# Optimization experiments

Measured on AMD Instinct MI355X. Metric: run time of the kernel, lower is better.

The kernel has to match this reference:

```python
import jax, jax.numpy as jnp
import numpy as np

# Config constants (mirror Qwen3_5TextConfig)
H = 1024        # hidden_size
I = 512         # moe_intermediate_size
IS = 2048       # shared_expert_intermediate_size
E = 16          # num_experts
TOP_K = 4       # num_experts_per_tok
NORM_TOPK = True
B, S = 1, 1024


def setup_inputs() -> dict:
    key = jax.random.key(0)
    ks = jax.random.split(key, 10)
    s = 0.02
    return {
        "hidden_states": jax.random.normal(ks[0], (B, S, H), jnp.float32),
        "w_router": (jax.random.normal(ks[1], (H, E), jnp.float32) * s),
        # stacked expert weights; Linear(H->I) stored as [E, H, I] for einsum
        "w_gate": (jax.random.normal(ks[2], (E, H, I), jnp.float32) * s),
        "w_up": (jax.random.normal(ks[3], (E, H, I), jnp.float32) * s),
        "w_down": (jax.random.normal(ks[4], (E, I, H), jnp.float32) * s),
        # shared expert (dense MLP)
        "ws_gate": (jax.random.normal(ks[5], (H, IS), jnp.float32) * s),
        "ws_up": (jax.random.normal(ks[6], (H, IS), jnp.float32) * s),
        "ws_down": (jax.random.normal(ks[7], (IS, H), jnp.float32) * s),
        "w_shared_gate": (jax.random.normal(ks[8], (H, 1), jnp.float32) * s),
    }


def reference(hidden_states, w_router, w_gate, w_up, w_down,
              ws_gate, ws_up, ws_down, w_shared_gate):
    b, sl, hd = hidden_states.shape
    x = hidden_states.reshape(-1, hd)              # [T, H]
    T = x.shape[0]

    # --- router: softmax in fp32, top-k, optional renormalization ---
    router_logits = x @ w_router                   # [T, E]
    probs = jax.nn.softmax(router_logits.astype(jnp.float32), axis=-1)
    top_w, top_i = jax.lax.top_k(probs, TOP_K)     # [T, K]
    if NORM_TOPK:
        top_w = top_w / top_w.sum(axis=-1, keepdims=True)
    # dense per-token expert weights (zeros off the top-k)
    dense_w = jnp.zeros((T, E), x.dtype).at[jnp.arange(T)[:, None], top_i].set(
        top_w.astype(x.dtype))                     # [T, E]

    # --- expert MLPs (SwiGLU), computed for all experts then masked-combined ---
    g = jnp.einsum('th,ehi->tei', x, w_gate)       # [T, E, I]
    u = jnp.einsum('th,ehi->tei', x, w_up)         # [T, E, I]
    expert_out = jnp.einsum('tei,eih->teh', jax.nn.silu(g) * u, w_down)  # [T, E, H]
    moe_out = jnp.einsum('te,teh->th', dense_w, expert_out)             # [T, H]

    # --- shared expert + sigmoid gate ---
    shared = (jax.nn.silu(x @ ws_gate) * (x @ ws_up)) @ ws_down          # [T, H]
    shared_gate = jax.nn.sigmoid(x @ w_shared_gate)                      # [T, 1]
    out = (moe_out + shared_gate * shared).reshape(b, sl, hd)
    return out, router_logits
```

## Files before the change

### kernel.cpp

```cpp
#include <hip/hip_runtime.h>
#include <hip/hip_bf16.h>

#define T_ 1024
#define H_ 1024
#define I_ 512
#define IS_ 2048
#define E_ 16

typedef __attribute__((ext_vector_type(8))) short short8;
typedef __attribute__((ext_vector_type(4))) float f32x4;

__device__ __forceinline__ unsigned short f2bf(float f) {
  unsigned u = __builtin_bit_cast(unsigned, f);
  unsigned r = (u + 0x7fffu + ((u >> 16) & 1u)) >> 16;
  return (unsigned short)r;
}

__device__ __forceinline__ void gload16(const void* g, void* l) {
  __builtin_amdgcn_global_load_lds(
      (const __attribute__((address_space(1))) unsigned int*)g,
      (__attribute__((address_space(3))) unsigned int*)l, 16, 0, 0);
}

__device__ __forceinline__ void transpose_cstrip(
    const float* __restrict__ src, unsigned short* __restrict__ dst,
    int C, int Rf, int r_start, int n0, int nch) {
  __shared__ unsigned short tile[2][64 * 66];
  int tid = threadIdx.x;
  int c = (tid & 15) << 2;
  int r0 = (tid >> 4) << 2;
  int orr = tid >> 2;
  int ks = (tid & 3) << 4;
  const float* sp0 = src + (long)(r_start + r0) * C + n0 + c;
  unsigned short* dbase = dst + (long)(n0 + orr) * Rf + r_start + ks;

  float4 va[4], vb[4];
#pragma unroll
  for (int r = 0; r < 4; r++) va[r] = *(const float4*)(sp0 + (long)r * C);

  for (int t = 0; t < nch; t += 2) {
    {
      const float* sp = sp0 + (long)(t + 1) * 64 * C;
#pragma unroll
      for (int r = 0; r < 4; r++) vb[r] = *(const float4*)(sp + (long)r * C);
    }
    {
      unsigned short* tb = &tile[0][0];
      ushort4 w;
      w = (ushort4){f2bf(va[0].x), f2bf(va[1].x), f2bf(va[2].x), f2bf(va[3].x)};
      *(ushort4*)&tb[(c + 0) * 66 + r0] = w;
      w = (ushort4){f2bf(va[0].y), f2bf(va[1].y), f2bf(va[2].y), f2bf(va[3].y)};
      *(ushort4*)&tb[(c + 1) * 66 + r0] = w;
      w = (ushort4){f2bf(va[0].z), f2bf(va[1].z), f2bf(va[2].z), f2bf(va[3].z)};
      *(ushort4*)&tb[(c + 2) * 66 + r0] = w;
      w = (ushort4){f2bf(va[0].w), f2bf(va[1].w), f2bf(va[2].w), f2bf(va[3].w)};
      *(ushort4*)&tb[(c + 3) * 66 + r0] = w;
      asm volatile("s_waitcnt lgkmcnt(0)" ::: "memory");
      __builtin_amdgcn_sched_barrier(0);
      __builtin_amdgcn_s_barrier();
      __builtin_amdgcn_sched_barrier(0);
      uint4 o0 = *(const uint4*)&tb[orr * 66 + ks];
      uint4 o1 = *(const uint4*)&tb[orr * 66 + ks + 8];
      unsigned short* d = dbase + (long)t * 64;
      *(uint4*)d = o0;
      *(uint4*)(d + 8) = o1;
    }
    if (t + 2 < nch) {
      const float* sp = sp0 + (long)(t + 2) * 64 * C;
#pragma unroll
      for (int r = 0; r < 4; r++) va[r] = *(const float4*)(sp + (long)r * C);
    }
    {
      unsigned short* tb = &tile[1][0];
      ushort4 w;
      w = (ushort4){f2bf(vb[0].x), f2bf(vb[1].x), f2bf(vb[2].x), f2bf(vb[3].x)};
      *(ushort4*)&tb[(c + 0) * 66 + r0] = w;
      w = (ushort4){f2bf(vb[0].y), f2bf(vb[1].y), f2bf(vb[2].y), f2bf(vb[3].y)};
      *(ushort4*)&tb[(c + 1) * 66 + r0] = w;
      w = (ushort4){f2bf(vb[0].z), f2bf(vb[1].z), f2bf(vb[2].z), f2bf(vb[3].z)};
      *(ushort4*)&tb[(c + 2) * 66 + r0] = w;
      w = (ushort4){f2bf(vb[0].w), f2bf(vb[1].w), f2bf(vb[2].w), f2bf(vb[3].w)};
      *(ushort4*)&tb[(c + 3) * 66 + r0] = w;
      asm volatile("s_waitcnt lgkmcnt(0)" ::: "memory");
      __builtin_amdgcn_sched_barrier(0);
      __builtin_amdgcn_s_barrier();
      __builtin_amdgcn_sched_barrier(0);
      uint4 o0 = *(const uint4*)&tb[orr * 66 + ks];
      uint4 o1 = *(const uint4*)&tb[orr * 66 + ks + 8];
      unsigned short* d = dbase + (long)(t + 1) * 64;
      *(uint4*)d = o0;
      *(uint4*)(d + 8) = o1;
    }
  }
}

__global__ __launch_bounds__(256) void k_router(
    const float* __restrict__ x, const float* __restrict__ wr,
    const float* __restrict__ wshg,
    unsigned short* __restrict__ xb, float* __restrict__ logits_out,
    int* __restrict__ top_i, float* __restrict__ top_w,
    float* __restrict__ gate_sig) {
  __shared__ float red[4][17];
  int t = blockIdx.x, tid = threadIdx.x;
  int h0 = tid << 2;
  float acc[17];
#pragma unroll
  for (int e = 0; e < 17; e++) acc[e] = 0.f;
  float4 xv = *(const float4*)(x + (long)t * H_ + h0);
  float4 wsh = *(const float4*)(wshg + h0);
  ushort4 xo;
  xo.x = f2bf(xv.x); xo.y = f2bf(xv.y); xo.z = f2bf(xv.z); xo.w = f2bf(xv.w);
  *(ushort4*)(xb + (long)t * H_ + h0) = xo;
  float xs[4] = {xv.x, xv.y, xv.z, xv.w};
  float ws[4] = {wsh.x, wsh.y, wsh.z, wsh.w};
#pragma unroll
  for (int j = 0; j < 4; j++) {
    const float4* w4 = (const float4*)(wr + (long)(h0 + j) * 16);
    float4 w0 = w4[0], w1 = w4[1], w2 = w4[2], w3 = w4[3];
    float xvj = xs[j];
    acc[0] += xvj * w0.x; acc[1] += xvj * w0.y; acc[2] += xvj * w0.z; acc[3] += xvj * w0.w;
    acc[4] += xvj * w1.x; acc[5] += xvj * w1.y; acc[6] += xvj * w1.z; acc[7] += xvj * w1.w;
    acc[8] += xvj * w2.x; acc[9] += xvj * w2.y; acc[10] += xvj * w2.z; acc[11] += xvj * w2.w;
    acc[12] += xvj * w3.x; acc[13] += xvj * w3.y; acc[14] += xvj * w3.z; acc[15] += xvj * w3.w;
    acc[16] += xvj * ws[j];
  }
#pragma unroll
  for (int off = 32; off >= 1; off >>= 1) {
#pragma unroll
    for (int e = 0; e < 17; e++) acc[e] += __shfl_xor(acc[e], off, 64);
  }
  int wid = tid >> 6, lane = tid & 63;
  if (lane == 0) {
#pragma unroll
    for (int e = 0; e < 17; e++) red[wid][e] = acc[e];
  }
  __syncthreads();
  if (tid == 0) {
    float a[17];
#pragma unroll
    for (int e = 0; e < 17; e++)
      a[e] = red[0][e] + red[1][e] + red[2][e] + red[3][e];
    float m = a[0];
#pragma unroll
    for (int e = 1; e < 16; e++) m = fmaxf(m, a[e]);
    float p[16], s = 0.f;
#pragma unroll
    for (int e = 0; e < 16; e++) { p[e] = expf(a[e] - m); s += p[e]; }
    float inv = 1.f / s;
#pragma unroll
    for (int e = 0; e < 16; e++) p[e] *= inv;
    int ti[4]; float tw[4]; float tsum = 0.f;
#pragma unroll
    for (int k = 0; k < 4; k++) {
      float best = -1.f; int bi = 0;
#pragma unroll
      for (int e = 0; e < 16; e++)
        if (p[e] > best) { best = p[e]; bi = e; }
      ti[k] = bi; tw[k] = best; tsum += best; p[bi] = -2.f;
    }
    float rn = 1.f / tsum;
#pragma unroll
    for (int e = 0; e < 16; e++) logits_out[(long)t * 16 + e] = a[e];
#pragma unroll
    for (int k = 0; k < 4; k++) {
      top_i[t * 4 + k] = ti[k];
      top_w[t * 4 + k] = tw[k] * rn;
    }
    gate_sig[t] = 1.f / (1.f + expf(-a[16]));
  }
}

__global__ __launch_bounds__(256) void k_wtb(
    const float* __restrict__ wg, const float* __restrict__ wu,
    const float* __restrict__ wd, const float* __restrict__ wsg,
    const float* __restrict__ wsu, const float* __restrict__ wsd,
    unsigned short* __restrict__ WGUT, unsigned short* __restrict__ WDT,
    unsigned short* __restrict__ WSGUT, unsigned short* __restrict__ WSDT,
    const int* __restrict__ top_i, const float* __restrict__ top_w,
    int* __restrict__ counts, int* __restrict__ offsets,
    int* __restrict__ perm, float* __restrict__ wslot,
    int* __restrict__ gu_tiles, int* __restrict__ dn_tiles,
    int* __restrict__ ntl) {
  int id = blockIdx.x;
  if (id < 960) {
    const float* src; unsigned short* dst; int C, Rf, r0s, n0, nch;
    if (id < 64) {
      int s = id >> 2, q = id & 3;
      src = wsd; dst = WSDT; C = H_; Rf = IS_;
      n0 = s * 64; r0s = q * 512; nch = 8;
    } else if (id < 128) {
      int l = id - 64, s = l >> 1, h = l & 1;
      src = wsg; dst = WSGUT; C = IS_; Rf = H_;
      n0 = s * 64; r0s = h * 512; nch = 8;
    } else if (id < 192) {
      int l = id - 128, s = l >> 1, h = l & 1;
      src = wsu; dst = WSGUT + (long)IS_ * H_; C = IS_; Rf = H_;
      n0 = s * 64; r0s = h * 512; nch = 8;
    } else if (id < 448) {
      int l = id - 192, e = l >> 4, s = (l >> 1) & 7, h = l & 1;
      src = wg + (long)e * H_ * I_; dst = WGUT + (long)e * 2 * I_ * H_;
      C = I_; Rf = H_; n0 = s * 64; r0s = h * 512; nch = 8;
    } else if (id < 704) {
      int l = id - 448, e = l >> 4, s = (l >> 1) & 7, h = l & 1;
      src = wu + (long)e * H_ * I_;
      dst = WGUT + (long)e * 2 * I_ * H_ + (long)I_ * H_;
      C = I_; Rf = H_; n0 = s * 64; r0s = h * 512; nch = 8;
    } else {
      int l = id - 704, e = l >> 4, s = l & 15;
      src = wd + (long)e * I_ * H_; dst = WDT + (long)e * H_ * I_;
      C = H_; Rf = I_; n0 = s * 64; r0s = 0; nch = 8;
    }
    transpose_cstrip(src, dst, C, Rf, r0s, n0, nch);
    return;
  }
  __shared__ int cnt[E_], cur[E_], mt[E_], pg[E_];
  int tid = threadIdx.x;
  if (tid < E_) cnt[tid] = 0;
  __syncthreads();
  for (int i = tid; i < T_ * 4; i += 256)
    atomicAdd(&cnt[top_i[i]], 1);
  __syncthreads();
  if (tid == 0) {
    int run = 0, trun = 0;
    for (int e = 0; e < E_; e++) {
      int c = cnt[e];
      counts[e] = c;
      offsets[e] = run;
      cur[e] = run;
      run += c;
      mt[e] = (c + 63) >> 6;
      pg[e] = trun;
      trun += mt[e];
    }
    ntl[0] = 512 + trun * 8;
    ntl[1] = 256 + trun * 16;
  }
  __syncthreads();
  for (int i = tid; i < T_ * 4; i += 256) {
    int e = top_i[i];
    int pos = atomicAdd(&cur[e], 1);
    perm[pos] = i >> 2;
    wslot[pos] = top_w[i];
  }
  for (int i = tid; i < 512; i += 256)
    gu_tiles[i] = ((i >> 5) << 6) | (i & 31);
  if (tid < 256)
    dn_tiles[tid] = ((tid >> 4) << 6) | (tid & 15);
  int trun = pg[E_ - 1] + mt[E_ - 1];
  for (int i = tid; i < trun * 8; i += 256) {
    int m = i >> 3, x = i & 7;
    int e = 0;
    while (e < E_ - 1 && m >= pg[e] + mt[e]) e++;
    int y = m - pg[e];
    gu_tiles[512 + i] = ((e + 1) << 12) | (y << 6) | x;
  }
  for (int i = tid; i < trun * 16; i += 256) {
    int m = i >> 4, x = i & 15;
    int e = 0;
    while (e < E_ - 1 && m >= pg[e] + mt[e]) e++;
    int y = m - pg[e];
    dn_tiles[256 + i] = ((e + 1) << 12) | (y << 6) | x;
  }
}

__global__ __launch_bounds__(256) void k_gemm_gu(
    const unsigned short* __restrict__ XB,
    const unsigned short* __restrict__ WSGUT, const unsigned short* __restrict__ WGUT,
    unsigned short* __restrict__ HSB, unsigned short* __restrict__ HB,
    const int* __restrict__ counts, const int* __restrict__ offsets,
    const int* __restrict__ perm, const int* __restrict__ gu_tiles,
    const int* __restrict__ ntl) {
  __shared__ unsigned short lds[3][6144];

  int tid = threadIdx.x, wid = tid >> 6, lane = tid & 63;
  int sub = lane >> 2;
  int ksw = ((lane & 3) ^ ((sub >> 1) & 3)) << 3;
  int soff = wid * 512;
  int fr = lane & 15, quad = lane >> 4;
  int fslot = (quad ^ ((fr >> 1) & 3)) << 3;
  int wm = (wid >> 1) * 32, wn = (wid & 1) * 32;

  int n_tiles = ntl[0];
  for (int w = blockIdx.x; w < n_tiles; w += gridDim.x) {
    int twd = gu_tiles[w];
    int z = twd >> 12;
    int mtile = ((twd >> 6) & 63) * 64;
    int ntile = (twd & 63) * 64;
    int M, row_base, uoff, ldd;
    const unsigned short* B0;
    unsigned short* DST;
    const int* pp;
    if (z == 0) {
      M = T_; row_base = 0; B0 = WSGUT; uoff = IS_;
      DST = HSB; ldd = IS_; pp = nullptr;
    } else {
      int e = z - 1;
      M = counts[e];
      row_base = offsets[e];
      B0 = WGUT + (long)e * 2 * I_ * H_;
      uoff = I_;
      DST = HB; ldd = I_; pp = perm;
    }

    int rm = mtile + wid * 16 + sub;
    if (rm > M - 1) rm = M - 1;
    long arow = pp ? (long)pp[row_base + rm] : (long)(row_base + rm);
    const unsigned short* aptr = XB + arow * H_ + ksw;
    int rbn = ntile + wid * 16 + sub;
    const unsigned short* bgptr = B0 + (long)rbn * H_ + ksw;
    const unsigned short* buptr = B0 + (long)(rbn + uoff) * H_ + ksw;

    f32x4 acc[2][2][2];
#pragma unroll
    for (int h = 0; h < 2; h++)
#pragma unroll
      for (int i = 0; i < 2; i++)
#pragma unroll
        for (int j = 0; j < 2; j++) acc[h][i][j] = (f32x4){0.f, 0.f, 0.f, 0.f};

    auto STAGE = [&](int slot, int kt) {
      int ko = kt * 32;
      unsigned short* base = &lds[slot][0];
      gload16(aptr + ko, base + soff);
      gload16(bgptr + ko, base + 2048 + soff);
      gload16(buptr + ko, base + 4096 + soff);
    };

    const int NK = H_ / 32;
    asm volatile("s_waitcnt lgkmcnt(0)" ::: "memory");
    __builtin_amdgcn_s_barrier();
    __builtin_amdgcn_sched_barrier(0);
    STAGE(0, 0);
    STAGE(1, 1);
    int cur = 0, stg = 2;
    for (int kt = 0; kt < NK; kt++) {
      if (kt + 1 < NK) asm volatile("s_waitcnt vmcnt(3)" ::: "memory");
      else             asm volatile("s_waitcnt vmcnt(0)" ::: "memory");
      __builtin_amdgcn_s_barrier();
      __builtin_amdgcn_sched_barrier(0);
      if (kt + 2 < NK) STAGE(stg, kt + 2);
      __builtin_amdgcn_sched_barrier(0);
      const unsigned short* As = &lds[cur][0];
      const unsigned short* Bg = &lds[cur][2048];
      const unsigned short* Bu = &lds[cur][4096];
      short8 af[2], bg[2], bu[2];
#pragma unroll
      for (int i = 0; i < 2; i++)
        af[i] = *(const short8*)(&As[(wm + i * 16 + fr) * 32 + fslot]);
#pragma unroll
      for (int j = 0; j < 2; j++) {
        bg[j] = *(const short8*)(&Bg[(wn + j * 16 + fr) * 32 + fslot]);
        bu[j] = *(const short8*)(&Bu[(wn + j * 16 + fr) * 32 + fslot]);
      }
#pragma unroll
      for (int i = 0; i < 2; i++)
#pragma unroll
        for (int j = 0; j < 2; j++) {
          acc[0][i][j] = __builtin_amdgcn_mfma_f32_16x16x32_bf16(af[i], bg[j], acc[0][i][j], 0, 0, 0);
          acc[1][i][j] = __builtin_amdgcn_mfma_f32_16x16x32_bf16(af[i], bu[j], acc[1][i][j], 0, 0, 0);
        }
      asm volatile("s_waitcnt lgkmcnt(0)" ::: "memory");
      __builtin_amdgcn_sched_barrier(0);
      cur = (cur == 2) ? 0 : cur + 1;
      stg = (stg == 2) ? 0 : stg + 1;
    }

#pragma unroll
    for (int i = 0; i < 2; i++) {
      int m0 = mtile + wm + i * 16 + quad * 4;
#pragma unroll
      for (int j = 0; j < 2; j++) {
        int col = ntile + wn + j * 16 + fr;
#pragma unroll
        for (int r = 0; r < 4; r++) {
          int m = m0 + r;
          if (m < M) {
            float g = acc[0][i][j][r], u = acc[1][i][j][r];
            DST[(long)(row_base + m) * ldd + col] = f2bf(g / (1.f + expf(-g)) * u);
          }
        }
      }
    }
  }
}

__global__ __launch_bounds__(256) void k_gemm_dn(
    const unsigned short* __restrict__ HSB, const unsigned short* __restrict__ WSDT,
    const unsigned short* __restrict__ HB, const unsigned short* __restrict__ WDT,
    const int* __restrict__ counts, const int* __restrict__ offsets,
    const int* __restrict__ perm, const float* __restrict__ wslot,
    const float* __restrict__ gate_sig,
    const int* __restrict__ dn_tiles, const int* __restrict__ ntl,
    float* __restrict__ out) {
  __shared__ unsigned short lds[3][4096];

  int tid = threadIdx.x, wid = tid >> 6, lane = tid & 63;
  int sub = lane >> 2;
  int ksw = ((lane & 3) ^ ((sub >> 1) & 3)) << 3;
  int soff = wid * 512;
  int fr = lane & 15, quad = lane >> 4;
  int fslot = (quad ^ ((fr >> 1) & 3)) << 3;
  int wm = (wid >> 1) * 32, wn = (wid & 1) * 32;

  int n_tiles = ntl[1];
  for (int w = blockIdx.x; w < n_tiles; w += gridDim.x) {
    int twd = dn_tiles[w];
    int z = twd >> 12;
    int mtile = ((twd >> 6) & 63) * 64;
    int ntile = (twd & 63) * 64;
    const unsigned short *A, *B;
    int K, M, rb;
    if (z == 0) {
      A = HSB; K = IS_; M = T_; rb = 0; B = WSDT;
    } else {
      int e = z - 1;
      M = counts[e];
      rb = offsets[e];
      A = HB; K = I_; B = WDT + (long)e * H_ * I_;
    }

    int rm = mtile + wid * 16 + sub;
    if (rm > M - 1) rm = M - 1;
    const unsigned short* aptr = A + (long)(rb + rm) * K + ksw;
    int rbn = ntile + wid * 16 + sub;
    const unsigned short* bptr = B + (long)rbn * K + ksw;

    f32x4 acc[2][2];
#pragma unroll
    for (int i = 0; i < 2; i++)
#pragma unroll
      for (int j = 0; j < 2; j++) acc[i][j] = (f32x4){0.f, 0.f, 0.f, 0.f};

    auto STAGE = [&](int slot, int kt) {
      int ko = kt * 32;
      unsigned short* base = &lds[slot][0];
      gload16(aptr + ko, base + soff);
      gload16(bptr + ko, base + 2048 + soff);
    };

    const int NK = K / 32;
    asm volatile("s_waitcnt lgkmcnt(0)" ::: "memory");
    __builtin_amdgcn_s_barrier();
    __builtin_amdgcn_sched_barrier(0);
    STAGE(0, 0);
    STAGE(1, 1);
    int cur = 0, stg = 2;
    for (int kt = 0; kt < NK; kt++) {
      if (kt + 1 < NK) asm volatile("s_waitcnt vmcnt(2)" ::: "memory");
      else             asm volatile("s_waitcnt vmcnt(0)" ::: "memory");
      __builtin_amdgcn_s_barrier();
      __builtin_amdgcn_sched_barrier(0);
      if (kt + 2 < NK) STAGE(stg, kt + 2);
      __builtin_amdgcn_sched_barrier(0);
      const unsigned short* As = &lds[cur][0];
      const unsigned short* Bs = &lds[cur][2048];
      short8 af[2], bf[2];
#pragma unroll
      for (int i = 0; i < 2; i++)
        af[i] = *(const short8*)(&As[(wm + i * 16 + fr) * 32 + fslot]);
#pragma unroll
      for (int j = 0; j < 2; j++)
        bf[j] = *(const short8*)(&Bs[(wn + j * 16 + fr) * 32 + fslot]);
#pragma unroll
      for (int i = 0; i < 2; i++)
#pragma unroll
        for (int j = 0; j < 2; j++)
          acc[i][j] = __builtin_amdgcn_mfma_f32_16x16x32_bf16(af[i], bf[j], acc[i][j], 0, 0, 0);
      asm volatile("s_waitcnt lgkmcnt(0)" ::: "memory");
      __builtin_amdgcn_sched_barrier(0);
      cur = (cur == 2) ? 0 : cur + 1;
      stg = (stg == 2) ? 0 : stg + 1;
    }

#pragma unroll
    for (int i = 0; i < 2; i++) {
      int m0 = mtile + wm + i * 16 + quad * 4;
#pragma unroll
      for (int j = 0; j < 2; j++) {
        int col = ntile + wn + j * 16 + fr;
#pragma unroll
        for (int r = 0; r < 4; r++) {
          int m = m0 + r;
          if (m < M) {
            if (z == 0) {
              float gs = gate_sig[m];
              atomicAdd(&out[(long)m * H_ + col], gs * acc[i][j][r]);
            } else {
              int tkn = perm[rb + m];
              float wgt = wslot[rb + m];
              atomicAdd(&out[(long)tkn * H_ + col], wgt * acc[i][j][r]);
            }
          }
        }
      }
    }
  }
}

extern "C" void kernel_launch(void* const* d_in, const int* in_sizes, int n_in,
                              void* d_out, int out_size, void* d_ws, size_t ws_size,
                              hipStream_t stream) {
  const float* x    = (const float*)d_in[0];
  const float* wrt  = (const float*)d_in[1];
  const float* wg   = (const float*)d_in[2];
  const float* wu   = (const float*)d_in[3];
  const float* wd   = (const float*)d_in[4];
  const float* wsg  = (const float*)d_in[5];
  const float* wsu  = (const float*)d_in[6];
  const float* wsd  = (const float*)d_in[7];
  const float* wshg = (const float*)d_in[8];
  float* out = (float*)d_out;
  float* logits_out = out + (long)T_ * H_;

  char* ws = (char*)d_ws;
  size_t off = 0;
  auto take = [&](size_t bytes) -> void* {
    void* p = ws + off;
    off += (bytes + 255) & ~(size_t)255;
    return p;
  };

  unsigned short* XB    = (unsigned short*)take((size_t)T_ * H_ * 2);
  unsigned short* WGUT  = (unsigned short*)take((size_t)E_ * 2 * I_ * H_ * 2);
  unsigned short* WDT   = (unsigned short*)take((size_t)E_ * H_ * I_ * 2);
  unsigned short* WSGUT = (unsigned short*)take((size_t)2 * IS_ * H_ * 2);
  unsigned short* WSDT  = (unsigned short*)take((size_t)H_ * IS_ * 2);
  unsigned short* HSB   = (unsigned short*)take((size_t)T_ * IS_ * 2);
  unsigned short* HB    = (unsigned short*)take((size_t)4096 * I_ * 2);
  int*   counts   = (int*)take(64);
  int*   offsets  = (int*)take(64);
  int*   top_i    = (int*)take((size_t)T_ * 4 * 4);
  float* top_w    = (float*)take((size_t)T_ * 4 * 4);
  int*   perm     = (int*)take((size_t)4096 * 4);
  float* wslot    = (float*)take((size_t)4096 * 4);
  float* gate_sig = (float*)take((size_t)T_ * 4);
  int*   gu_tiles = (int*)take((size_t)2048 * 4);
  int*   dn_tiles = (int*)take((size_t)2048 * 4);
  int*   ntl      = (int*)take(64);

  k_router<<<T_, 256, 0, stream>>>(x, wrt, wshg, XB, logits_out,
                                   top_i, top_w, gate_sig);
  k_wtb<<<961, 256, 0, stream>>>(wg, wu, wd, wsg, wsu, wsd,
                                 WGUT, WDT, WSGUT, WSDT,
                                 top_i, top_w, counts, offsets, perm, wslot,
                                 gu_tiles, dn_tiles, ntl);
  k_gemm_gu<<<1024, 256, 0, stream>>>(XB, WSGUT, WGUT, HSB, HB,
                                      counts, offsets, perm, gu_tiles, ntl);
  k_gemm_dn<<<1280, 256, 0, stream>>>(HSB, WSDT, HB, WDT,
                                      counts, offsets, perm, wslot, gate_sig,
                                      dn_tiles, ntl, out);
}
```

Baseline: 264.9 us.

## Enlarge GEMM M-tile to 128 rows with per-wave 32x64 output blocks

Both grouped GEMM kernels move from 64x64 to 128x64 output tiles. Each wave now owns 32 rows across all 64 columns, loading two A rows per stage and sharing the B fragments. Tile counts, tile-list encoding and grid sizes are adjusted to match. This raises arithmetic intensity and cuts redundant weight loads. The cost is more LDS and registers per block, fewer tiles to spread across CUs, and more padding waste for experts with few tokens.

```diff
diff --git a/kernel.cpp b/kernel.cpp
--- a/kernel.cpp
+++ b/kernel.cpp
@@ -228,12 +228,12 @@
       offsets[e] = run;
       cur[e] = run;
       run += c;
-      mt[e] = (c + 63) >> 6;
+      mt[e] = (c + 127) >> 7;
       pg[e] = trun;
       trun += mt[e];
     }
-    ntl[0] = 512 + trun * 8;
-    ntl[1] = 256 + trun * 16;
+    ntl[0] = 256 + trun * 8;
+    ntl[1] = 128 + trun * 16;
   }
   __syncthreads();
   for (int i = tid; i < T_ * 4; i += 256) {
@@ -242,24 +242,24 @@
     perm[pos] = i >> 2;
     wslot[pos] = top_w[i];
   }
-  for (int i = tid; i < 512; i += 256)
-    gu_tiles[i] = ((i >> 5) << 6) | (i & 31);
   if (tid < 256)
+    gu_tiles[tid] = ((tid >> 5) << 6) | (tid & 31);
+  if (tid < 128)
     dn_tiles[tid] = ((tid >> 4) << 6) | (tid & 15);
   int trun = pg[E_ - 1] + mt[E_ - 1];
   for (int i = tid; i < trun * 8; i += 256) {
-    int m = i >> 3, x = i & 7;
+    int m = i >> 3, xx = i & 7;
     int e = 0;
     while (e < E_ - 1 && m >= pg[e] + mt[e]) e++;
     int y = m - pg[e];
-    gu_tiles[512 + i] = ((e + 1) << 12) | (y << 6) | x;
+    gu_tiles[256 + i] = ((e + 1) << 12) | (y << 6) | xx;
   }
   for (int i = tid; i < trun * 16; i += 256) {
-    int m = i >> 4, x = i & 15;
+    int m = i >> 4, xx = i & 15;
     int e = 0;
     while (e < E_ - 1 && m >= pg[e] + mt[e]) e++;
     int y = m - pg[e];
-    dn_tiles[256 + i] = ((e + 1) << 12) | (y << 6) | x;
+    dn_tiles[128 + i] = ((e + 1) << 12) | (y << 6) | xx;
   }
 }
 
@@ -270,21 +270,19 @@
     const int* __restrict__ counts, const int* __restrict__ offsets,
     const int* __restrict__ perm, const int* __restrict__ gu_tiles,
     const int* __restrict__ ntl) {
-  __shared__ unsigned short lds[3][6144];
+  __shared__ unsigned short lds[3][8192];
 
   int tid = threadIdx.x, wid = tid >> 6, lane = tid & 63;
   int sub = lane >> 2;
   int ksw = ((lane & 3) ^ ((sub >> 1) & 3)) << 3;
-  int soff = wid * 512;
   int fr = lane & 15, quad = lane >> 4;
   int fslot = (quad ^ ((fr >> 1) & 3)) << 3;
-  int wm = (wid >> 1) * 32, wn = (wid & 1) * 32;
 
   int n_tiles = ntl[0];
   for (int w = blockIdx.x; w < n_tiles; w += gridDim.x) {
     int twd = gu_tiles[w];
     int z = twd >> 12;
-    int mtile = ((twd >> 6) & 63) * 64;
+    int mtile = ((twd >> 6) & 63) * 128;
     int ntile = (twd & 63) * 64;
     int M, row_base, uoff, ldd;
     const unsigned short* B0;
@@ -302,31 +300,150 @@
       DST = HB; ldd = I_; pp = perm;
     }
 
-    int rm = mtile + wid * 16 + sub;
-    if (rm > M - 1) rm = M - 1;
-    long arow = pp ? (long)pp[row_base + rm] : (long)(row_base + rm);
-    const unsigned short* aptr = XB + arow * H_ + ksw;
+    int r0 = mtile + wid * 32 + sub;
+    int r1 = r0 + 16;
+    if (r0 > M - 1) r0 = M - 1;
+    if (r1 > M - 1) r1 = M - 1;
+    long a0 = pp ? (long)pp[row_base + r0] : (long)(row_base + r0);
+    long a1 = pp ? (long)pp[row_base + r1] : (long)(row_base + r1);
+    const unsigned short* aptr0 = XB + a0 * H_ + ksw;
+    const unsigned short* aptr1 = XB + a1 * H_ + ksw;
     int rbn = ntile + wid * 16 + sub;
     const unsigned short* bgptr = B0 + (long)rbn * H_ + ksw;
     const unsigned short* buptr = B0 + (long)(rbn + uoff) * H_ + ksw;
 
-    f32x4 acc[2][2][2];
+    f32x4 acc[2][2][4];
 #pragma unroll
     for (int h = 0; h < 2; h++)
 #pragma unroll
       for (int i = 0; i < 2; i++)
 #pragma unroll
-        for (int j = 0; j < 2; j++) acc[h][i][j] = (f32x4){0.f, 0.f, 0.f, 0.f};
+        for (int j = 0; j < 4; j++) acc[h][i][j] = (f32x4){0.f, 0.f, 0.f, 0.f};
 
     auto STAGE = [&](int slot, int kt) {
       int ko = kt * 32;
       unsigned short* base = &lds[slot][0];
-      gload16(aptr + ko, base + soff);
-      gload16(bgptr + ko, base + 2048 + soff);
-      gload16(buptr + ko, base + 4096 + soff);
+      gload16(aptr0 + ko, base + wid * 1024);
+      gload16(aptr1 + ko, base + wid * 1024 + 512);
+      gload16(bgptr + ko, base + 4096 + wid * 512);
+      gload16(buptr + ko, base + 6144 + wid * 512);
     };
 
     const int NK = H_ / 32;
+    asm volatile("s_waitcnt lgkmcnt(0)" ::: "memory");
+    __builtin_amdgcn_s_barrier();
+    __builtin_amdgcn_sched_barrier(0);
+    STAGE(0, 0);
+    STAGE(1, 1);
+    int cur = 0, stg = 2;
+    for (int kt = 0; kt < NK; kt++) {
+      if (kt + 1 < NK) asm volatile("s_waitcnt vmcnt(4)" ::: "memory");
+      else             asm volatile("s_waitcnt vmcnt(0)" ::: "memory");
+      __builtin_amdgcn_s_barrier();
+      __builtin_amdgcn_sched_barrier(0);
+      if (kt + 2 < NK) STAGE(stg, kt + 2);
+      __builtin_amdgcn_sched_barrier(0);
+      const unsigned short* As = &lds[cur][0];
+      const unsigned short* Bg = &lds[cur][4096];
+      const unsigned short* Bu = &lds[cur][6144];
+      short8 af[2], bg[4], bu[4];
+#pragma unroll
+      for (int i = 0; i < 2; i++)
+        af[i] = *(const short8*)(&As[(wid * 32 + i * 16 + fr) * 32 + fslot]);
+#pragma unroll
+      for (int j = 0; j < 4; j++) {
+        bg[j] = *(const short8*)(&Bg[(j * 16 + fr) * 32 + fslot]);
+        bu[j] = *(const short8*)(&Bu[(j * 16 + fr) * 32 + fslot]);
+      }
+#pragma unroll
+      for (int i = 0; i < 2; i++)
+#pragma unroll
+        for (int j = 0; j < 4; j++) {
+          acc[0][i][j] = __builtin_amdgcn_mfma_f32_16x16x32_bf16(af[i], bg[j], acc[0][i][j], 0, 0, 0);
+          acc[1][i][j] = __builtin_amdgcn_mfma_f32_16x16x32_bf16(af[i], bu[j], acc[1][i][j], 0, 0, 0);
+        }
+      asm volatile("s_waitcnt lgkmcnt(0)" ::: "memory");
+      __builtin_amdgcn_sched_barrier(0);
+      cur = (cur == 2) ? 0 : cur + 1;
+      stg = (stg == 2) ? 0 : stg + 1;
+    }
+
+#pragma unroll
+    for (int i = 0; i < 2; i++) {
+      int m0 = mtile + wid * 32 + i * 16 + quad * 4;
+#pragma unroll
+      for (int j = 0; j < 4; j++) {
+        int col = ntile + j * 16 + fr;
+#pragma unroll
+        for (int r = 0; r < 4; r++) {
+          int m = m0 + r;
+          if (m < M) {
+            float g = acc[0][i][j][r], u = acc[1][i][j][r];
+            DST[(long)(row_base + m) * ldd + col] = f2bf(g / (1.f + expf(-g)) * u);
+          }
+        }
+      }
+    }
+  }
+}
+
+__global__ __launch_bounds__(256) void k_gemm_dn(
+    const unsigned short* __restrict__ HSB, const unsigned short* __restrict__ WSDT,
+    const unsigned short* __restrict__ HB, const unsigned short* __restrict__ WDT,
+    const int* __restrict__ counts, const int* __restrict__ offsets,
+    const int* __restrict__ perm, const float* __restrict__ wslot,
+    const float* __restrict__ gate_sig,
+    const int* __restrict__ dn_tiles, const int* __restrict__ ntl,
+    float* __restrict__ out) {
+  __shared__ unsigned short lds[3][6144];
+
+  int tid = threadIdx.x, wid = tid >> 6, lane = tid & 63;
+  int sub = lane >> 2;
+  int ksw = ((lane & 3) ^ ((sub >> 1) & 3)) << 3;
+  int fr = lane & 15, quad = lane >> 4;
+  int fslot = (quad ^ ((fr >> 1) & 3)) << 3;
+
+  int n_tiles = ntl[1];
+  for (int w = blockIdx.x; w < n_tiles; w += gridDim.x) {
+    int twd = dn_tiles[w];
+    int z = twd >> 12;
+    int mtile = ((twd >> 6) & 63) * 128;
+    int ntile = (twd & 63) * 64;
+    const unsigned short *A, *B;
+    int K, M, rb;
+    if (z == 0) {
+      A = HSB; K = IS_; M = T_; rb = 0; B = WSDT;
+    } else {
+      int e = z - 1;
+      M = counts[e];
+      rb = offsets[e];
+      A = HB; K = I_; B = WDT + (long)e * H_ * I_;
+    }
+
+    int r0 = mtile + wid * 32 + sub;
+    int r1 = r0 + 16;
+    if (r0 > M - 1) r0 = M - 1;
+    if (r1 > M - 1) r1 = M - 1;
+    const unsigned short* aptr0 = A + (long)(rb + r0) * K + ksw;
+    const unsigned short* aptr1 = A + (long)(rb + r1) * K + ksw;
+    int rbn = ntile + wid * 16 + sub;
+    const unsigned short* bptr = B + (long)rbn * K + ksw;
+
+    f32x4 acc[2][4];
+#pragma unroll
+    for (int i = 0; i < 2; i++)
+#pragma unroll
+      for (int j = 0; j < 4; j++) acc[i][j] = (f32x4){0.f, 0.f, 0.f, 0.f};
+
+    auto STAGE = [&](int slot, int kt) {
+      int ko = kt * 32;
+      unsigned short* base = &lds[slot][0];
+      gload16(aptr0 + ko, base + wid * 1024);
+      gload16(aptr1 + ko, base + wid * 1024 + 512);
+      gload16(bptr + ko, base + 4096 + wid * 512);
+    };
+
+    const int NK = K / 32;
     asm volatile("s_waitcnt lgkmcnt(0)" ::: "memory");
     __builtin_amdgcn_s_barrier();
     __builtin_amdgcn_sched_barrier(0);
@@ -341,24 +458,19 @@
       if (kt + 2 < NK) STAGE(stg, kt + 2);
       __builtin_amdgcn_sched_barrier(0);
       const unsigned short* As = &lds[cur][0];
-      const unsigned short* Bg = &lds[cur][2048];
-      const unsigned short* Bu = &lds[cur][4096];
-      short8 af[2], bg[2], bu[2];
+      const unsigned short* Bs = &lds[cur][4096];
+      short8 af[2], bf[4];
 #pragma unroll
       for (int i = 0; i < 2; i++)
-        af[i] = *(const short8*)(&As[(wm + i * 16 + fr) * 32 + fslot]);
-#pragma unroll
-      for (int j = 0; j < 2; j++) {
-        bg[j] = *(const short8*)(&Bg[(wn + j * 16 + fr) * 32 + fslot]);
-        bu[j] = *(const short8*)(&Bu[(wn + j * 16 + fr) * 32 + fslot]);
-      }
+        af[i] = *(const short8*)(&As[(wid * 32 + i * 16 + fr) * 32 + fslot]);
+#pragma unroll
+      for (int j = 0; j < 4; j++)
+        bf[j] = *(const short8*)(&Bs[(j * 16 + fr) * 32 + fslot]);
 #pragma unroll
       for (int i = 0; i < 2; i++)
 #pragma unroll
-        for (int j = 0; j < 2; j++) {
-          acc[0][i][j] = __builtin_amdgcn_mfma_f32_16x16x32_bf16(af[i], bg[j], acc[0][i][j], 0, 0, 0);
-          acc[1][i][j] = __builtin_amdgcn_mfma_f32_16x16x32_bf16(af[i], bu[j], acc[1][i][j], 0, 0, 0);
-        }
+        for (int j = 0; j < 4; j++)
+          acc[i][j] = __builtin_amdgcn_mfma_f32_16x16x32_bf16(af[i], bf[j], acc[i][j], 0, 0, 0);
       asm volatile("s_waitcnt lgkmcnt(0)" ::: "memory");
       __builtin_amdgcn_sched_barrier(0);
       cur = (cur == 2) ? 0 : cur + 1;
@@ -367,117 +479,10 @@
 
 #pragma unroll
     for (int i = 0; i < 2; i++) {
-      int m0 = mtile + wm + i * 16 + quad * 4;
-#pragma unroll
-      for (int j = 0; j < 2; j++) {
-        int col = ntile + wn + j * 16 + fr;
-#pragma unroll
-        for (int r = 0; r < 4; r++) {
-          int m = m0 + r;
-          if (m < M) {
-            float g = acc[0][i][j][r], u = acc[1][i][j][r];
-            DST[(long)(row_base + m) * ldd + col] = f2bf(g / (1.f + expf(-g)) * u);
-          }
-        }
-      }
-    }
-  }
-}
-
-__global__ __launch_bounds__(256) void k_gemm_dn(
-    const unsigned short* __restrict__ HSB, const unsigned short* __restrict__ WSDT,
-    const unsigned short* __restrict__ HB, const unsigned short* __restrict__ WDT,
-    const int* __restrict__ counts, const int* __restrict__ offsets,
-    const int* __restrict__ perm, const float* __restrict__ wslot,
-    const float* __restrict__ gate_sig,
-    const int* __restrict__ dn_tiles, const int* __restrict__ ntl,
-    float* __restrict__ out) {
-  __shared__ unsigned short lds[3][4096];
-
-  int tid = threadIdx.x, wid = tid >> 6, lane = tid & 63;
-  int sub = lane >> 2;
-  int ksw = ((lane & 3) ^ ((sub >> 1) & 3)) << 3;
-  int soff = wid * 512;
-  int fr = lane & 15, quad = lane >> 4;
-  int fslot = (quad ^ ((fr >> 1) & 3)) << 3;
-  int wm = (wid >> 1) * 32, wn = (wid & 1) * 32;
-
-  int n_tiles = ntl[1];
-  for (int w = blockIdx.x; w < n_tiles; w += gridDim.x) {
-    int twd = dn_tiles[w];
-    int z = twd >> 12;
-    int mtile = ((twd >> 6) & 63) * 64;
-    int ntile = (twd & 63) * 64;
-    const unsigned short *A, *B;
-    int K, M, rb;
-    if (z == 0) {
-      A = HSB; K = IS_; M = T_; rb = 0; B = WSDT;
-    } else {
-      int e = z - 1;
-      M = counts[e];
-      rb = offsets[e];
-      A = HB; K = I_; B = WDT + (long)e * H_ * I_;
-    }
-
-    int rm = mtile + wid * 16 + sub;
-    if (rm > M - 1) rm = M - 1;
-    const unsigned short* aptr = A + (long)(rb + rm) * K + ksw;
-    int rbn = ntile + wid * 16 + sub;
-    const unsigned short* bptr = B + (long)rbn * K + ksw;
-
-    f32x4 acc[2][2];
-#pragma unroll
-    for (int i = 0; i < 2; i++)
-#pragma unroll
-      for (int j = 0; j < 2; j++) acc[i][j] = (f32x4){0.f, 0.f, 0.f, 0.f};
-
-    auto STAGE = [&](int slot, int kt) {
-      int ko = kt * 32;
-      unsigned short* base = &lds[slot][0];
-      gload16(aptr + ko, base + soff);
-      gload16(bptr + ko, base + 2048 + soff);
-    };
-
-    const int NK = K / 32;
-    asm volatile("s_waitcnt lgkmcnt(0)" ::: "memory");
-    __builtin_amdgcn_s_barrier();
-    __builtin_amdgcn_sched_barrier(0);
-    STAGE(0, 0);
-    STAGE(1, 1);
-    int cur = 0, stg = 2;
-    for (int kt = 0; kt < NK; kt++) {
-      if (kt + 1 < NK) asm volatile("s_waitcnt vmcnt(2)" ::: "memory");
-      else             asm volatile("s_waitcnt vmcnt(0)" ::: "memory");
-      __builtin_amdgcn_s_barrier();
-      __builtin_amdgcn_sched_barrier(0);
-      if (kt + 2 < NK) STAGE(stg, kt + 2);
-      __builtin_amdgcn_sched_barrier(0);
-      const unsigned short* As = &lds[cur][0];
-      const unsigned short* Bs = &lds[cur][2048];
-      short8 af[2], bf[2];
-#pragma unroll
-      for (int i = 0; i < 2; i++)
-        af[i] = *(const short8*)(&As[(wm + i * 16 + fr) * 32 + fslot]);
-#pragma unroll
-      for (int j = 0; j < 2; j++)
-        bf[j] = *(const short8*)(&Bs[(wn + j * 16 + fr) * 32 + fslot]);
-#pragma unroll
-      for (int i = 0; i < 2; i++)
-#pragma unroll
-        for (int j = 0; j < 2; j++)
-          acc[i][j] = __builtin_amdgcn_mfma_f32_16x16x32_bf16(af[i], bf[j], acc[i][j], 0, 0, 0);
-      asm volatile("s_waitcnt lgkmcnt(0)" ::: "memory");
-      __builtin_amdgcn_sched_barrier(0);
-      cur = (cur == 2) ? 0 : cur + 1;
-      stg = (stg == 2) ? 0 : stg + 1;
-    }
-
-#pragma unroll
-    for (int i = 0; i < 2; i++) {
-      int m0 = mtile + wm + i * 16 + quad * 4;
-#pragma unroll
-      for (int j = 0; j < 2; j++) {
-        int col = ntile + wn + j * 16 + fr;
+      int m0 = mtile + wid * 32 + i * 16 + quad * 4;
+#pragma unroll
+      for (int j = 0; j < 4; j++) {
+        int col = ntile + j * 16 + fr;
 #pragma unroll
         for (int r = 0; r < 4; r++) {
           int m = m0 + r;
@@ -544,9 +549,9 @@
                                  WGUT, WDT, WSGUT, WSDT,
                                  top_i, top_w, counts, offsets, perm, wslot,
                                  gu_tiles, dn_tiles, ntl);
-  k_gemm_gu<<<1024, 256, 0, stream>>>(XB, WSGUT, WGUT, HSB, HB,
-                                      counts, offsets, perm, gu_tiles, ntl);
-  k_gemm_dn<<<1280, 256, 0, stream>>>(HSB, WSDT, HB, WDT,
-                                      counts, offsets, perm, wslot, gate_sig,
-                                      dn_tiles, ntl, out);
-}
+  k_gemm_gu<<<640, 256, 0, stream>>>(XB, WSGUT, WGUT, HSB, HB,
+                                     counts, offsets, perm, gu_tiles, ntl);
+  k_gemm_dn<<<640, 256, 0, stream>>>(HSB, WSDT, HB, WDT,
+                                     counts, offsets, perm, wslot, gate_sig,
+                                     dn_tiles, ntl, out);
+}
```

After: 280.1 us. 1.06x slower.
